# Performance work log

Hardware: AMD Instinct MI355X
Metric: run time of the kernel (lower is better)

Reference implementation:

```python
import jax, jax.numpy as jnp
import numpy as np

HEADS = 16


def setup_inputs() -> dict:
    key = jax.random.key(0)
    ks = jax.random.split(key, 6)
    b, n, c = 4, 2048, 1024  # batch, seq_len, query_dim (== hidden_dim)
    h = 1024                 # hidden_dim = heads * dim_head = 16 * 64
    s = 0.02
    return {
        "x": jax.random.normal(ks[0], (b, n, c), jnp.float32),
        "Wq": jax.random.normal(ks[1], (h, c), jnp.float32) * s,
        "Wk": jax.random.normal(ks[2], (h, c), jnp.float32) * s,
        "Wv": jax.random.normal(ks[3], (h, c), jnp.float32) * s,
        "Wout": jax.random.normal(ks[4], (c, h), jnp.float32) * s,
        "bout": jnp.zeros((c,), jnp.float32),
    }


def reference(x, Wq, Wk, Wv, Wout, bout):
    # x: (b, n, c). Self-attention (context = x).
    b, n, c = x.shape
    m = HEADS
    d = Wq.shape[0] // m  # dim_head
    # 1x1 conv == linear projection over channel dim
    q = jnp.einsum('bnc,hc->bnh', x, Wq).reshape(b, n, m, d)
    k = jnp.einsum('bnc,hc->bnh', x, Wk).reshape(b, n, m, d)
    v = jnp.einsum('bnc,hc->bnh', x, Wv).reshape(b, n, m, d)
    scale = d ** (-0.25)  # 1/sqrt(sqrt(d)), applied to both q and k
    # weight: (b, m, n_q, n_k)
    weight = jnp.einsum('bimd,bjmd->bmij', q * scale, k * scale)
    weight = jax.nn.softmax(weight, axis=-1)
    a = jnp.einsum('bmij,bjmd->bimd', weight, v).reshape(b, n, m * d)
    return jnp.einsum('bnh,ch->bnc', a, Wout) + bout
```

## Files before the change

### kernel.cpp

```cpp
#include <hip/hip_runtime.h>
#include <stdint.h>
#include <stddef.h>

typedef __attribute__((ext_vector_type(4))) float f32x4;
typedef __attribute__((ext_vector_type(16))) float f32x16;
typedef __attribute__((ext_vector_type(8))) short s16x8;
typedef __attribute__((ext_vector_type(4))) short s16x4;

__device__ __forceinline__ short f2bf(float f) {
  uint32_t u = __builtin_bit_cast(uint32_t, f);
  uint32_t r = (u + 0x7fffu + ((u >> 16) & 1u)) >> 16;
  return (short)r;
}

__device__ __forceinline__ void gload_lds16(const void* g, void* l) {
  __builtin_amdgcn_global_load_lds(
      (const __attribute__((address_space(1))) void*)g,
      (__attribute__((address_space(3))) void*)l, 16, 0, 0);
}

__device__ __forceinline__ int msk8(int r) { return (r & 7) ^ ((r >> 3) & 7); }
__device__ __forceinline__ int swz(int r, int c) {
  return r * 64 + (c ^ (msk8(r) << 3));
}

__global__ __launch_bounds__(256) void cvt_kernel(const float* __restrict__ src,
                                                  short* __restrict__ dst, int n4) {
  int i = blockIdx.x * blockDim.x + threadIdx.x;
  if (i >= n4) return;
  float4 v = reinterpret_cast<const float4*>(src)[i];
  s16x4 o;
  o[0] = f2bf(v.x); o[1] = f2bf(v.y); o[2] = f2bf(v.z); o[3] = f2bf(v.w);
  reinterpret_cast<s16x4*>(dst)[i] = o;
}

template <int OUTF32>
__global__ __launch_bounds__(256) void gemm_bt(const short* __restrict__ A,
                                               const short* __restrict__ B,
                                               void* __restrict__ Cv,
                                               const float* __restrict__ bias,
                                               int M, int N, int K) {
  __shared__ short lA[128 * 64];
  __shared__ short lB[128 * 64];
  const int tid = threadIdx.x;
  const int lane = tid & 63, wid = tid >> 6;
  const int g = lane >> 4, li = lane & 15;
  const int nbx = N >> 7;
  const int by = blockIdx.x / nbx, bx = blockIdx.x % nbx;
  const int brow = by << 7, bcol = bx << 7;
  const int wr = (wid >> 1) << 6, wc = (wid & 1) << 6;

  f32x4 acc[4][4] = {};

  for (int k0 = 0; k0 < K; k0 += 64) {
    __syncthreads();
#pragma unroll
    for (int i = 0; i < 4; i++) {
      int j = tid + i * 256;
      int r = j >> 3, s = j & 7;
      gload_lds16(A + (size_t)(brow + r) * K + k0 + 8 * (s ^ msk8(r)), &lA[j * 8]);
    }
#pragma unroll
    for (int i = 0; i < 4; i++) {
      int j = tid + i * 256;
      int r = j >> 3, s = j & 7;
      gload_lds16(B + (size_t)(bcol + r) * K + k0 + 8 * (s ^ msk8(r)), &lB[j * 8]);
    }
    __syncthreads();
#pragma unroll
    for (int ks = 0; ks < 2; ks++) {
      s16x8 af[4], bfr[4];
#pragma unroll
      for (int ai = 0; ai < 4; ai++) {
        int row = wr + ai * 16 + li;
        af[ai] = *(const s16x8*)&lA[swz(row, ks * 32 + g * 8)];
      }
#pragma unroll
      for (int bj = 0; bj < 4; bj++) {
        int row = wc + bj * 16 + li;
        bfr[bj] = *(const s16x8*)&lB[swz(row, ks * 32 + g * 8)];
      }
#pragma unroll
      for (int ai = 0; ai < 4; ai++)
#pragma unroll
        for (int bj = 0; bj < 4; bj++)
          acc[ai][bj] = __builtin_amdgcn_mfma_f32_16x16x32_bf16(af[ai], bfr[bj],
                                                               acc[ai][bj], 0, 0, 0);
    }
  }

#pragma unroll
  for (int ai = 0; ai < 4; ai++) {
#pragma unroll
    for (int bj = 0; bj < 4; bj++) {
#pragma unroll
      for (int e = 0; e < 4; e++) {
        int row = brow + wr + ai * 16 + g * 4 + e;
        int col = bcol + wc + bj * 16 + li;
        float v = acc[ai][bj][e];
        if (OUTF32) {
          ((float*)Cv)[(size_t)row * N + col] = v + bias[col];
        } else {
          ((short*)Cv)[(size_t)row * N + col] = f2bf(v);
        }
      }
    }
  }
}

__global__ __launch_bounds__(256, 3) void attn_kernel(const short* __restrict__ qkv,
                                                      short* __restrict__ aout) {
  __shared__ short lQ[4 * 4 * 512];
  __shared__ short lK[4 * 512];
  __shared__ short lV[4 * 512];

  const int tid = threadIdx.x;
  const int lane = tid & 63, w = tid >> 6;
  const int l31 = lane & 31, hi = lane >> 5;
  const int bid = blockIdx.x;
  const int qt = bid & 15, head = (bid >> 4) & 15, b = bid >> 8;
  const int row0 = b * 2048;
  const int qrow = qt * 128 + w * 32 + l31;
  const int qcol = head * 64, kcol = 1024 + head * 64, vcol = 2048 + head * 64;

#pragma unroll
  for (int s = 0; s < 4; s++)
    gload_lds16(qkv + (size_t)(row0 + qrow) * 3072 + qcol + 16 * s + 8 * hi,
                &lQ[(w * 4 + s) * 512]);
  __syncthreads();
  s16x8 qf[4];
#pragma unroll
  for (int s = 0; s < 4; s++)
    qf[s] = *(const s16x8*)&lQ[(w * 4 + s) * 512 + lane * 8];

  const int vj = tid >> 3, va = tid & 7;
  const int vdd = va >> 2, va3 = va & 3;
  const int vhi = (vj >> 3) & 1, vks = vj >> 4, vef = vj & 7;
  const int vblk = (vks * 2 + vdd) * 512;
  const int vxor = va3 | (vhi << 2);
  const int vslot_r = (lane ^ ((lane >> 3) & 7)) * 8;

  f32x16 acc0 = {}, acc1 = {};
  float m2 = -1e30f, l_r = 0.f;
  const float SCL = 0.125f * 1.44269504088896f;
  const float THR = 8.f * 1.44269504088896f;

  for (int jt = 0; jt < 64; jt++) {
    const int jbase = jt * 32;
    s16x8 vstage =
        *(const s16x8*)(qkv + (size_t)(row0 + jbase + vj) * 3072 + vcol + 8 * va);
    __syncthreads();
    gload_lds16(qkv + (size_t)(row0 + jbase + l31) * 3072 + kcol + 16 * w + 8 * hi,
                &lK[w * 512]);
#pragma unroll
    for (int t2 = 0; t2 < 8; t2++) {
      int slot = 32 * vhi + 8 * va3 + (t2 ^ vxor);
      lV[vblk + slot * 8 + vef] = vstage[t2];
    }
    __syncthreads();

    f32x16 st = {};
#pragma unroll
    for (int s = 0; s < 4; s++) {
      s16x8 kf = *(const s16x8*)&lK[s * 512 + lane * 8];
      st = __builtin_amdgcn_mfma_f32_32x32x16_bf16(kf, qf[s], st, 0, 0, 0);
    }

    float scl[16];
#pragma unroll
    for (int r = 0; r < 16; r++) scl[r] = st[r] * SCL;
    float pm = scl[0];
#pragma unroll
    for (int r = 1; r < 16; r++) pm = fmaxf(pm, scl[r]);
    pm = fmaxf(pm, __shfl_xor(pm, 32, 64));
    if (__any(pm > m2 + THR)) {
      float mn = fmaxf(m2, pm);
      float al = exp2f(m2 - mn);
      m2 = mn;
      l_r *= al;
#pragma unroll
      for (int r = 0; r < 16; r++) { acc0[r] *= al; acc1[r] *= al; }
    }
    float p[16];
    float rs = 0.f;
#pragma unroll
    for (int r = 0; r < 16; r++) { p[r] = exp2f(scl[r] - m2); rs += p[r]; }
    rs += __shfl_xor(rs, 32, 64);
    l_r += rs;

#pragma unroll
    for (int ks = 0; ks < 2; ks++) {
      int x0, x1, y0, y1;
      asm("v_cvt_pk_bf16_f32 %0, %1, %2" : "=v"(x0) : "v"(p[8*ks+0]), "v"(p[8*ks+1]));
      asm("v_cvt_pk_bf16_f32 %0, %1, %2" : "=v"(x1) : "v"(p[8*ks+2]), "v"(p[8*ks+3]));
      asm("v_cvt_pk_bf16_f32 %0, %1, %2" : "=v"(y0) : "v"(p[8*ks+4]), "v"(p[8*ks+5]));
      asm("v_cvt_pk_bf16_f32 %0, %1, %2" : "=v"(y1) : "v"(p[8*ks+6]), "v"(p[8*ks+7]));
      int sx0 = __shfl_xor(x0, 32, 64);
      int sx1 = __shfl_xor(x1, 32, 64);
      int sy0 = __shfl_xor(y0, 32, 64);
      int sy1 = __shfl_xor(y1, 32, 64);
      int4 paw;
      paw.x = hi ? sy0 : x0;
      paw.y = hi ? sy1 : x1;
      paw.z = hi ? y0 : sx0;
      paw.w = hi ? y1 : sx1;
      s16x8 pa = __builtin_bit_cast(s16x8, paw);
      s16x8 v0 = *(const s16x8*)&lV[(ks * 2 + 0) * 512 + vslot_r];
      s16x8 v1 = *(const s16x8*)&lV[(ks * 2 + 1) * 512 + vslot_r];
      acc0 = __builtin_amdgcn_mfma_f32_32x32x16_bf16(v0, pa, acc0, 0, 0, 0);
      acc1 = __builtin_amdgcn_mfma_f32_32x32x16_bf16(v1, pa, acc1, 0, 0, 0);
    }
  }

  float inv = 1.f / l_r;
  const size_t rowoff = (size_t)(row0 + qt * 128 + w * 32 + l31) * 1024 + head * 64;
#pragma unroll
  for (int r = 0; r < 16; r++) {
    int dbase = (r & 3) + 8 * (r >> 2) + 4 * hi;
    aout[rowoff + dbase] = f2bf(acc0[r] * inv);
    aout[rowoff + 32 + dbase] = f2bf(acc1[r] * inv);
  }
}

extern "C" void kernel_launch(void* const* d_in, const int* in_sizes, int n_in,
                              void* d_out, int out_size, void* d_ws, size_t ws_size,
                              hipStream_t stream) {
  const float* x    = (const float*)d_in[0];
  const float* Wq   = (const float*)d_in[1];
  const float* Wk   = (const float*)d_in[2];
  const float* Wv   = (const float*)d_in[3];
  const float* Wout = (const float*)d_in[4];
  const float* bout = (const float*)d_in[5];
  float* out = (float*)d_out;

  char* ws = (char*)d_ws;
  short* xb    = (short*)(ws);
  short* Wqkv  = (short*)(ws + (16ull << 20));
  short* Woutb = (short*)(ws + (22ull << 20));
  short* qkv   = (short*)(ws + (24ull << 20));
  short* a_ws  = xb;

  cvt_kernel<<<8192, 256, 0, stream>>>(x, xb, 2097152);
  cvt_kernel<<<1024, 256, 0, stream>>>(Wq, Wqkv, 262144);
  cvt_kernel<<<1024, 256, 0, stream>>>(Wk, Wqkv + 1048576, 262144);
  cvt_kernel<<<1024, 256, 0, stream>>>(Wv, Wqkv + 2097152, 262144);
  cvt_kernel<<<1024, 256, 0, stream>>>(Wout, Woutb, 262144);

  gemm_bt<0><<<64 * 24, 256, 0, stream>>>(xb, Wqkv, qkv, nullptr, 8192, 3072, 1024);

  attn_kernel<<<1024, 256, 0, stream>>>(qkv, a_ws);

  gemm_bt<1><<<64 * 8, 256, 0, stream>>>(a_ws, Woutb, out, bout, 8192, 1024, 1024);
}
```

Measured before the change: 318.8 us.

## Double-buffer attention K/V tiles, widen to 64 keys, fold softmax scale into QKV GEMM

The attention kernel now double-buffers K/V tiles in LDS, prefetching the next 64-key tile while the current one is computed, and processes two 32-key sub-tiles per iteration. This halves the loop trips and barrier count. The softmax scale (with log2e) is folded into the Q columns in the QKV GEMM epilogue, and permlane32_swap replaces the shuffle-and-select exchange. GEMM block indices are remapped with an XCD-aware swizzle, and attention occupancy is raised to 4. The risks are register pressure at the higher occupancy and a small precision change from scaling Q before the bf16 rounding.

```diff
diff --git a/kernel.cpp b/kernel.cpp
--- a/kernel.cpp
+++ b/kernel.cpp
@@ -6,6 +6,7 @@
 typedef __attribute__((ext_vector_type(16))) float f32x16;
 typedef __attribute__((ext_vector_type(8))) short s16x8;
 typedef __attribute__((ext_vector_type(4))) short s16x4;
+typedef __attribute__((ext_vector_type(2))) int i32x2;
 
 __device__ __forceinline__ short f2bf(float f) {
   uint32_t u = __builtin_bit_cast(uint32_t, f);
@@ -39,14 +40,18 @@
                                                const short* __restrict__ B,
                                                void* __restrict__ Cv,
                                                const float* __restrict__ bias,
-                                               int M, int N, int K) {
+                                               int M, int N, int K,
+                                               float qscl, int qcols) {
   __shared__ short lA[128 * 64];
   __shared__ short lB[128 * 64];
   const int tid = threadIdx.x;
   const int lane = tid & 63, wid = tid >> 6;
   const int g = lane >> 4, li = lane & 15;
   const int nbx = N >> 7;
-  const int by = blockIdx.x / nbx, bx = blockIdx.x % nbx;
+  const int q8 = gridDim.x >> 3;
+  const int orig = blockIdx.x;
+  const int bswz = (orig & 7) * q8 + (orig >> 3);
+  const int by = bswz / nbx, bx = bswz % nbx;
   const int brow = by << 7, bcol = bx << 7;
   const int wr = (wid >> 1) << 6, wc = (wid & 1) << 6;
 
@@ -98,6 +103,7 @@
         int row = brow + wr + ai * 16 + g * 4 + e;
         int col = bcol + wc + bj * 16 + li;
         float v = acc[ai][bj][e];
+        if (col < qcols) v *= qscl;
         if (OUTF32) {
           ((float*)Cv)[(size_t)row * N + col] = v + bias[col];
         } else {
@@ -108,11 +114,9 @@
   }
 }
 
-__global__ __launch_bounds__(256, 3) void attn_kernel(const short* __restrict__ qkv,
+__global__ __launch_bounds__(256, 4) void attn_kernel(const short* __restrict__ qkv,
                                                       short* __restrict__ aout) {
-  __shared__ short lQ[4 * 4 * 512];
-  __shared__ short lK[4 * 512];
-  __shared__ short lV[4 * 512];
+  __shared__ short lds[2][8192];
 
   const int tid = threadIdx.x;
   const int lane = tid & 63, w = tid >> 6;
@@ -126,12 +130,13 @@
 #pragma unroll
   for (int s = 0; s < 4; s++)
     gload_lds16(qkv + (size_t)(row0 + qrow) * 3072 + qcol + 16 * s + 8 * hi,
-                &lQ[(w * 4 + s) * 512]);
+                &lds[0][(w * 4 + s) * 512]);
   __syncthreads();
   s16x8 qf[4];
 #pragma unroll
   for (int s = 0; s < 4; s++)
-    qf[s] = *(const s16x8*)&lQ[(w * 4 + s) * 512 + lane * 8];
+    qf[s] = *(const s16x8*)&lds[0][(w * 4 + s) * 512 + lane * 8];
+  __syncthreads();
 
   const int vj = tid >> 3, va = tid & 7;
   const int vdd = va >> 2, va3 = va & 3;
@@ -140,38 +145,56 @@
   const int vxor = va3 | (vhi << 2);
   const int vslot_r = (lane ^ ((lane >> 3) & 7)) * 8;
 
+#pragma unroll
+  for (int sub = 0; sub < 2; sub++)
+    gload_lds16(qkv + (size_t)(row0 + sub * 32 + l31) * 3072 + kcol + 16 * w + 8 * hi,
+                &lds[0][(sub * 4 + w) * 512]);
+#pragma unroll
+  for (int sub = 0; sub < 2; sub++) {
+    s16x8 v0 = *(const s16x8*)(qkv + (size_t)(row0 + sub * 32 + vj) * 3072 + vcol + 8 * va);
+#pragma unroll
+    for (int t2 = 0; t2 < 8; t2++) {
+      int slot = 32 * vhi + 8 * va3 + (t2 ^ vxor);
+      lds[0][4096 + sub * 2048 + vblk + slot * 8 + vef] = v0[t2];
+    }
+  }
+  __syncthreads();
+
   f32x16 acc0 = {}, acc1 = {};
   float m2 = -1e30f, l_r = 0.f;
-  const float SCL = 0.125f * 1.44269504088896f;
   const float THR = 8.f * 1.44269504088896f;
 
-  for (int jt = 0; jt < 64; jt++) {
-    const int jbase = jt * 32;
-    s16x8 vstage =
-        *(const s16x8*)(qkv + (size_t)(row0 + jbase + vj) * 3072 + vcol + 8 * va);
-    __syncthreads();
-    gload_lds16(qkv + (size_t)(row0 + jbase + l31) * 3072 + kcol + 16 * w + 8 * hi,
-                &lK[w * 512]);
-#pragma unroll
-    for (int t2 = 0; t2 < 8; t2++) {
-      int slot = 32 * vhi + 8 * va3 + (t2 ^ vxor);
-      lV[vblk + slot * 8 + vef] = vstage[t2];
-    }
-    __syncthreads();
-
-    f32x16 st = {};
+  for (int jt = 0; jt < 32; jt++) {
+    const int cur = jt & 1, nxt = cur ^ 1;
+    const int jnext = (jt + 1) * 64;
+    const bool pf = (jt < 31);
+
+    s16x8 vs0, vs1;
+    if (pf) {
+      vs0 = *(const s16x8*)(qkv + (size_t)(row0 + jnext + vj) * 3072 + vcol + 8 * va);
+      vs1 = *(const s16x8*)(qkv + (size_t)(row0 + jnext + 32 + vj) * 3072 + vcol + 8 * va);
+#pragma unroll
+      for (int sub = 0; sub < 2; sub++)
+        gload_lds16(qkv + (size_t)(row0 + jnext + sub * 32 + l31) * 3072 + kcol +
+                        16 * w + 8 * hi,
+                    &lds[nxt][(sub * 4 + w) * 512]);
+    }
+
+    f32x16 st0 = {}, st1 = {};
+    const short* lc = &lds[cur][0];
 #pragma unroll
     for (int s = 0; s < 4; s++) {
-      s16x8 kf = *(const s16x8*)&lK[s * 512 + lane * 8];
-      st = __builtin_amdgcn_mfma_f32_32x32x16_bf16(kf, qf[s], st, 0, 0, 0);
-    }
-
-    float scl[16];
-#pragma unroll
-    for (int r = 0; r < 16; r++) scl[r] = st[r] * SCL;
-    float pm = scl[0];
-#pragma unroll
-    for (int r = 1; r < 16; r++) pm = fmaxf(pm, scl[r]);
+      s16x8 kf0 = *(const s16x8*)&lc[s * 512 + lane * 8];
+      s16x8 kf1 = *(const s16x8*)&lc[(4 + s) * 512 + lane * 8];
+      st0 = __builtin_amdgcn_mfma_f32_32x32x16_bf16(kf0, qf[s], st0, 0, 0, 0);
+      st1 = __builtin_amdgcn_mfma_f32_32x32x16_bf16(kf1, qf[s], st1, 0, 0, 0);
+    }
+
+    float pm = fmaxf(st0[0], st0[1]);
+#pragma unroll
+    for (int r = 2; r < 16; r++) pm = fmaxf(pm, st0[r]);
+#pragma unroll
+    for (int r = 0; r < 16; r++) pm = fmaxf(pm, st1[r]);
     pm = fmaxf(pm, __shfl_xor(pm, 32, 64));
     if (__any(pm > m2 + THR)) {
       float mn = fmaxf(m2, pm);
@@ -181,35 +204,46 @@
 #pragma unroll
       for (int r = 0; r < 16; r++) { acc0[r] *= al; acc1[r] *= al; }
     }
-    float p[16];
     float rs = 0.f;
 #pragma unroll
-    for (int r = 0; r < 16; r++) { p[r] = exp2f(scl[r] - m2); rs += p[r]; }
+    for (int r = 0; r < 16; r++) { st0[r] = exp2f(st0[r] - m2); rs += st0[r]; }
+#pragma unroll
+    for (int r = 0; r < 16; r++) { st1[r] = exp2f(st1[r] - m2); rs += st1[r]; }
     rs += __shfl_xor(rs, 32, 64);
     l_r += rs;
 
-#pragma unroll
-    for (int ks = 0; ks < 2; ks++) {
-      int x0, x1, y0, y1;
-      asm("v_cvt_pk_bf16_f32 %0, %1, %2" : "=v"(x0) : "v"(p[8*ks+0]), "v"(p[8*ks+1]));
-      asm("v_cvt_pk_bf16_f32 %0, %1, %2" : "=v"(x1) : "v"(p[8*ks+2]), "v"(p[8*ks+3]));
-      asm("v_cvt_pk_bf16_f32 %0, %1, %2" : "=v"(y0) : "v"(p[8*ks+4]), "v"(p[8*ks+5]));
-      asm("v_cvt_pk_bf16_f32 %0, %1, %2" : "=v"(y1) : "v"(p[8*ks+6]), "v"(p[8*ks+7]));
-      int sx0 = __shfl_xor(x0, 32, 64);
-      int sx1 = __shfl_xor(x1, 32, 64);
-      int sy0 = __shfl_xor(y0, 32, 64);
-      int sy1 = __shfl_xor(y1, 32, 64);
-      int4 paw;
-      paw.x = hi ? sy0 : x0;
-      paw.y = hi ? sy1 : x1;
-      paw.z = hi ? y0 : sx0;
-      paw.w = hi ? y1 : sx1;
-      s16x8 pa = __builtin_bit_cast(s16x8, paw);
-      s16x8 v0 = *(const s16x8*)&lV[(ks * 2 + 0) * 512 + vslot_r];
-      s16x8 v1 = *(const s16x8*)&lV[(ks * 2 + 1) * 512 + vslot_r];
-      acc0 = __builtin_amdgcn_mfma_f32_32x32x16_bf16(v0, pa, acc0, 0, 0, 0);
-      acc1 = __builtin_amdgcn_mfma_f32_32x32x16_bf16(v1, pa, acc1, 0, 0, 0);
-    }
+    if (pf) {
+#pragma unroll
+      for (int t2 = 0; t2 < 8; t2++) {
+        int slot = 32 * vhi + 8 * va3 + (t2 ^ vxor);
+        lds[nxt][4096 + vblk + slot * 8 + vef] = vs0[t2];
+        lds[nxt][4096 + 2048 + vblk + slot * 8 + vef] = vs1[t2];
+      }
+    }
+
+    const short* lV = &lds[cur][4096];
+#pragma unroll
+    for (int sub = 0; sub < 2; sub++) {
+      const float* p = sub ? (const float*)&st1 : (const float*)&st0;
+#pragma unroll
+      for (int ks = 0; ks < 2; ks++) {
+        int x0, x1, y0, y1;
+        asm("v_cvt_pk_bf16_f32 %0, %1, %2" : "=v"(x0) : "v"(p[8*ks+0]), "v"(p[8*ks+1]));
+        asm("v_cvt_pk_bf16_f32 %0, %1, %2" : "=v"(x1) : "v"(p[8*ks+2]), "v"(p[8*ks+3]));
+        asm("v_cvt_pk_bf16_f32 %0, %1, %2" : "=v"(y0) : "v"(p[8*ks+4]), "v"(p[8*ks+5]));
+        asm("v_cvt_pk_bf16_f32 %0, %1, %2" : "=v"(y1) : "v"(p[8*ks+6]), "v"(p[8*ks+7]));
+        i32x2 s02 = __builtin_amdgcn_permlane32_swap(x0, y0, false, false);
+        i32x2 s13 = __builtin_amdgcn_permlane32_swap(x1, y1, false, false);
+        int4 paw; paw.x = s02[0]; paw.y = s13[0]; paw.z = s02[1]; paw.w = s13[1];
+        s16x8 pa = __builtin_bit_cast(s16x8, paw);
+        s16x8 v0 = *(const s16x8*)&lV[sub * 2048 + (ks * 2 + 0) * 512 + vslot_r];
+        s16x8 v1 = *(const s16x8*)&lV[sub * 2048 + (ks * 2 + 1) * 512 + vslot_r];
+        acc0 = __builtin_amdgcn_mfma_f32_32x32x16_bf16(v0, pa, acc0, 0, 0, 0);
+        acc1 = __builtin_amdgcn_mfma_f32_32x32x16_bf16(v1, pa, acc1, 0, 0, 0);
+      }
+    }
+
+    __syncthreads();
   }
 
   float inv = 1.f / l_r;
@@ -240,15 +274,19 @@
   short* qkv   = (short*)(ws + (24ull << 20));
   short* a_ws  = xb;
 
+  const float SCL = 0.125f * 1.44269504088896f;
+
   cvt_kernel<<<8192, 256, 0, stream>>>(x, xb, 2097152);
   cvt_kernel<<<1024, 256, 0, stream>>>(Wq, Wqkv, 262144);
   cvt_kernel<<<1024, 256, 0, stream>>>(Wk, Wqkv + 1048576, 262144);
   cvt_kernel<<<1024, 256, 0, stream>>>(Wv, Wqkv + 2097152, 262144);
   cvt_kernel<<<1024, 256, 0, stream>>>(Wout, Woutb, 262144);
 
-  gemm_bt<0><<<64 * 24, 256, 0, stream>>>(xb, Wqkv, qkv, nullptr, 8192, 3072, 1024);
+  gemm_bt<0><<<64 * 24, 256, 0, stream>>>(xb, Wqkv, qkv, nullptr, 8192, 3072, 1024,
+                                          SCL, 1024);
 
   attn_kernel<<<1024, 256, 0, stream>>>(qkv, a_ws);
 
-  gemm_bt<1><<<64 * 8, 256, 0, stream>>>(a_ws, Woutb, out, bout, 8192, 1024, 1024);
-}
+  gemm_bt<1><<<64 * 8, 256, 0, stream>>>(a_ws, Woutb, out, bout, 8192, 1024, 1024,
+                                         1.f, 0);
+}
```

Result: faster. 300.3 us (-5.8%).
